# Kernel optimization log

Measured on AMD Instinct MI355X. Metric: run time of the kernel, lower is better.

## Reference

```python
import jax, jax.numpy as jnp
import numpy as np

B, D, N, H = 16384, 8, 64, 128   # batch, input_path_dim, cde_state_dim, vf_hidden_dim
NSIG = D + D * (D - 1) // 2       # Lyndon words up to depth 2: letters + pairs i<j


def setup_inputs() -> dict:
    key = jax.random.key(0)
    ks = jax.random.split(key, 6)
    g = lambda k, shape, scale: jax.random.normal(k, shape, jnp.float32) * scale
    return {
        "h": jax.random.normal(ks[0], (B, N), jnp.float32),
        "primitive_signature": jax.random.normal(ks[1], (B, NSIG), jnp.float32) * 0.1,
        "W1": g(ks[2], (H, N), (1.0 / N) ** 0.5),
        "b1": jnp.zeros((H,), jnp.float32),
        "W2": g(ks[3], (H, H), (1.0 / H) ** 0.5),
        "b2": jnp.zeros((H,), jnp.float32),
        "W3": g(ks[4], (D * N, H), (1.0 / H) ** 0.5),
        "b3": jnp.zeros((D * N,), jnp.float32),
    }


def reference(h, primitive_signature, W1, b1, W2, b2, W3, b3):
    d, n = D, N
    iu, ju = np.triu_indices(d, k=1)  # level-2 Lyndon words ij with i<j, lex order

    def vf(hv):  # MLP vector field: (n,) -> (d, n), one field per input channel
        z = jax.nn.softplus(W1 @ hv + b1)
        z = jax.nn.softplus(W2 @ z + b2)
        return jnp.tanh(W3 @ z + b3).reshape(d, n)

    def single(hv, sig):
        V = vf(hv)  # (d, n) level-1 brackets (the vector fields themselves)
        # JVP of the whole stacked field in direction t: J_{V_j}(h) @ t for all j
        jvp_dir = lambda t: jax.jvp(vf, (hv,), (t,))[1]  # (d, n)
        JV = jax.vmap(jvp_dir)(V)                         # (i, j, n) = J_{V_j} V_i
        # Lie bracket [V_i, V_j](h) = J_{V_j} V_i - J_{V_i} V_j
        br2 = JV - jnp.swapaxes(JV, 0, 1)                 # (i, j, n)
        lyn2 = br2[iu, ju]                                # (d*(d-1)/2, n)
        # log-ODE contraction: sum_w logsig_w * bracket_w(h)
        return sig[:d] @ V + sig[d:] @ lyn2               # (n,)

    return jax.vmap(single)(h, primitive_signature)
```

## Files before the change

kernel.cpp:

```cpp
#include <hip/hip_runtime.h>
#include <hip/hip_bf16.h>

#define NEL 16384

#define W1B_OFF 0
#define W2B_OFF 8192
#define W3B_OFF 24576
#define WS_WEIGHTS 90112
#define S1_OFF  90112
#define S2_OFF  (S1_OFF + NEL*128)
#define Z2_OFF  (S2_OFF + NEL*128)
#define V_OFF   (Z2_OFF + NEL*128)
#define DZ1_OFF (V_OFF + NEL*512)
#define DZ2_OFF (DZ1_OFF + NEL*8*128)

typedef __attribute__((ext_vector_type(8))) short bf16x8;
typedef __attribute__((ext_vector_type(4))) float f32x4;

__device__ __forceinline__ float bf2f(unsigned int u16) {
    unsigned int x = u16 << 16;
    float f; __builtin_memcpy(&f, &x, 4); return f;
}
__device__ __forceinline__ unsigned short f2bf(float f) {
    unsigned int x; __builtin_memcpy(&x, &f, 4);
    x = (x + 0x7FFFu + ((x >> 16) & 1u)) >> 16;
    return (unsigned short)x;
}
__device__ __forceinline__ void unpack8(uint4 q, float* f) {
    f[0] = bf2f(q.x & 0xFFFFu); f[1] = bf2f(q.x >> 16);
    f[2] = bf2f(q.y & 0xFFFFu); f[3] = bf2f(q.y >> 16);
    f[4] = bf2f(q.z & 0xFFFFu); f[5] = bf2f(q.z >> 16);
    f[6] = bf2f(q.w & 0xFFFFu); f[7] = bf2f(q.w >> 16);
}
__device__ __forceinline__ void sp_sig(float x, float& sp, float& sig) {
    float t = __expf(-fabsf(x));
    float r = __builtin_amdgcn_rcpf(1.f + t);
    sig = (x >= 0.f) ? r : 1.f - r;
    sp  = fmaxf(x, 0.f) + __logf(1.f + t);
}
__device__ __forceinline__ float tanh_fast(float x) {
    float t = __expf(-2.f * fabsf(x));
    float y = (1.f - t) * __builtin_amdgcn_rcpf(1.f + t);
    unsigned int xb, yb;
    __builtin_memcpy(&xb, &x, 4);
    __builtin_memcpy(&yb, &y, 4);
    yb |= (xb & 0x80000000u);
    float rr; __builtin_memcpy(&rr, &yb, 4);
    return rr;
}
__device__ __forceinline__ bf16x8 ldfrag(const unsigned short* p) {
    return *reinterpret_cast<const bf16x8*>(p);
}
__device__ __forceinline__ void cpu4(unsigned short* dst, const unsigned short* src) {
    *reinterpret_cast<uint4*>(dst) = *reinterpret_cast<const uint4*>(src);
}

__global__ void prep_weights(const float* __restrict__ W1,
                             const float* __restrict__ W2,
                             const float* __restrict__ W3,
                             unsigned short* __restrict__ wb) {
    int i = blockIdx.x * blockDim.x + threadIdx.x;
    if (i >= WS_WEIGHTS) return;
    float v;
    if (i < W2B_OFF) v = W1[i];
    else if (i < W3B_OFF) v = W2[i - W2B_OFF];
    else v = W3[i - W3B_OFF];
    wb[i] = f2bf(v);
}

#define K1_LDS 52224
__global__ __launch_bounds__(256, 2)
void k1_fwd12(const float* __restrict__ hg,
              const float* __restrict__ b1,
              const float* __restrict__ b2,
              unsigned short* __restrict__ wsb) {
    __shared__ __align__(16) char sm[K1_LDS];
    unsigned short* w1s = (unsigned short*)(sm);
    unsigned short* hs  = (unsigned short*)(sm + 18432);
    unsigned short* w2s = (unsigned short*)(sm);
    unsigned short* z1s = (unsigned short*)(sm + 34816);
    unsigned short* S1g = wsb + S1_OFF;
    unsigned short* S2g = wsb + S2_OFF;
    unsigned short* Z2g = wsb + Z2_OFF;

    const int tid = threadIdx.x;
    const int e0 = blockIdx.x * 64;
    const int lane = tid & 63;
    const int w = tid >> 6;
    const int r16 = lane & 15;
    const int kb = lane >> 4;

    #pragma unroll
    for (int q = 0; q < 4; ++q) {
        int idx = q * 256 + tid;
        int row = idx >> 3, u4 = idx & 7;
        cpu4(&w1s[row * 72 + u4 * 8], &wsb[W1B_OFF + row * 64 + u4 * 8]);
    }
    #pragma unroll
    for (int q = 0; q < 16; ++q) {
        int idx = q * 256 + tid;
        int row = idx >> 6, k = idx & 63;
        hs[row * 72 + k] = f2bf(hg[(e0 + row) * 64 + k]);
    }
    __syncthreads();

    {
        const unsigned short* Ab = hs + (w * 16 + r16) * 72 + kb * 8;
        bf16x8 a0 = ldfrag(Ab), a1 = ldfrag(Ab + 32);
        f32x4 acc[8] = {};
        #pragma unroll
        for (int nt = 0; nt < 8; ++nt) {
            const unsigned short* Bb = w1s + (nt * 16 + r16) * 72 + kb * 8;
            acc[nt] = __builtin_amdgcn_mfma_f32_16x16x32_bf16(a0, ldfrag(Bb), acc[nt], 0, 0, 0);
            acc[nt] = __builtin_amdgcn_mfma_f32_16x16x32_bf16(a1, ldfrag(Bb + 32), acc[nt], 0, 0, 0);
        }
        int rbase = w * 16 + kb * 4;
        #pragma unroll
        for (int nt = 0; nt < 8; ++nt) {
            int col = nt * 16 + r16;
            float bb = b1[col];
            #pragma unroll
            for (int rr = 0; rr < 4; ++rr) {
                float sp, sg;
                sp_sig(acc[nt][rr] + bb, sp, sg);
                z1s[(rbase + rr) * 136 + col] = f2bf(sp);
                S1g[(e0 + rbase + rr) * 128 + col] = f2bf(sg);
            }
        }
    }
    __syncthreads();

    #pragma unroll
    for (int q = 0; q < 8; ++q) {
        int idx = q * 256 + tid;
        int row = idx >> 4, u4 = idx & 15;
        cpu4(&w2s[row * 136 + u4 * 8], &wsb[W2B_OFF + row * 128 + u4 * 8]);
    }
    __syncthreads();

    {
        const unsigned short* Ab = z1s + (w * 16 + r16) * 136 + kb * 8;
        bf16x8 a[4];
        #pragma unroll
        for (int ks = 0; ks < 4; ++ks) a[ks] = ldfrag(Ab + ks * 32);
        f32x4 acc[8] = {};
        #pragma unroll
        for (int nt = 0; nt < 8; ++nt) {
            const unsigned short* Bb = w2s + (nt * 16 + r16) * 136 + kb * 8;
            #pragma unroll
            for (int ks = 0; ks < 4; ++ks)
                acc[nt] = __builtin_amdgcn_mfma_f32_16x16x32_bf16(a[ks], ldfrag(Bb + ks * 32), acc[nt], 0, 0, 0);
        }
        int rbase = w * 16 + kb * 4;
        #pragma unroll
        for (int nt = 0; nt < 8; ++nt) {
            int col = nt * 16 + r16;
            float bb = b2[col];
            #pragma unroll
            for (int rr = 0; rr < 4; ++rr) {
                float sp, sg;
                sp_sig(acc[nt][rr] + bb, sp, sg);
                Z2g[(e0 + rbase + rr) * 128 + col] = f2bf(sp);
                S2g[(e0 + rbase + rr) * 128 + col] = f2bf(sg);
            }
        }
    }
}

#define K2_LDS 52224
__global__ __launch_bounds__(256, 2)
void k2_fwd3(const float* __restrict__ b3,
             unsigned short* __restrict__ wsb) {
    __shared__ __align__(16) char sm[K2_LDS];
    unsigned short* z2s = (unsigned short*)(sm);
    unsigned short* wc  = (unsigned short*)(sm + 17408);
    const unsigned short* Z2g = wsb + Z2_OFF;
    unsigned short* Vg = wsb + V_OFF;

    const int tid = threadIdx.x;
    const int e0 = blockIdx.x * 64;
    const int lane = tid & 63;
    const int w = tid >> 6;
    const int r16 = lane & 15;
    const int kb = lane >> 4;

    #pragma unroll
    for (int q = 0; q < 4; ++q) {
        int idx = q * 256 + tid;
        int row = idx >> 4, u4 = idx & 15;
        cpu4(&z2s[row * 136 + u4 * 8], &Z2g[(e0 + row) * 128 + u4 * 8]);
    }

    for (int nc = 0; nc < 4; ++nc) {
        __syncthreads();
        #pragma unroll
        for (int q = 0; q < 8; ++q) {
            int idx = q * 256 + tid;
            int row = idx >> 4, u4 = idx & 15;
            cpu4(&wc[row * 136 + u4 * 8], &wsb[W3B_OFF + (nc * 128 + row) * 128 + u4 * 8]);
        }
        __syncthreads();

        const unsigned short* Ab = z2s + (w * 16 + r16) * 136 + kb * 8;
        bf16x8 a[4];
        #pragma unroll
        for (int ks = 0; ks < 4; ++ks) a[ks] = ldfrag(Ab + ks * 32);
        f32x4 acc[8] = {};
        #pragma unroll
        for (int nt = 0; nt < 8; ++nt) {
            const unsigned short* Bb = wc + (nt * 16 + r16) * 136 + kb * 8;
            #pragma unroll
            for (int ks = 0; ks < 4; ++ks)
                acc[nt] = __builtin_amdgcn_mfma_f32_16x16x32_bf16(a[ks], ldfrag(Bb + ks * 32), acc[nt], 0, 0, 0);
        }
        int rbase = w * 16 + kb * 4;
        #pragma unroll
        for (int nt = 0; nt < 8; ++nt) {
            int c = nc * 128 + nt * 16 + r16;
            float bb = b3[c];
            #pragma unroll
            for (int rr = 0; rr < 4; ++rr) {
                float v = tanh_fast(acc[nt][rr] + bb);
                Vg[(e0 + rbase + rr) * 512 + c] = f2bf(v);
            }
        }
    }
}

#define K3A_LDS 37120
__global__ __launch_bounds__(256, 4)
void k3a_jvp1(const float* __restrict__ sigg,
              unsigned short* __restrict__ wsb) {
    __shared__ __align__(16) char sm[K3A_LDS];
    unsigned short* vs  = (unsigned short*)(sm);
    unsigned short* w1s = (unsigned short*)(sm + 8320);
    unsigned short* ts  = (unsigned short*)(sm + 26752);
    float* sigsm = (float*)(sm + 35968);
    const unsigned short* S1g = wsb + S1_OFF;
    const unsigned short* Vg  = wsb + V_OFF;
    unsigned short* DZ1g = wsb + DZ1_OFF;

    const int tid = threadIdx.x;
    const int e0 = blockIdx.x * 8;
    const int lane = tid & 63;
    const int w = tid >> 6;
    const int r16 = lane & 15;
    const int kb = lane >> 4;

    #pragma unroll
    for (int q = 0; q < 2; ++q) {
        int idx = q * 256 + tid;
        int row = idx >> 6, u4 = idx & 63;
        cpu4(&vs[row * 520 + u4 * 8], &Vg[(e0 + row) * 512 + u4 * 8]);
    }
    #pragma unroll
    for (int q = 0; q < 4; ++q) {
        int idx = q * 256 + tid;
        int row = idx >> 3, u4 = idx & 7;
        cpu4(&w1s[row * 72 + u4 * 8], &wsb[W1B_OFF + row * 64 + u4 * 8]);
    }
    #pragma unroll
    for (int q = 0; q < 2; ++q) {
        int idx = q * 256 + tid;
        if (idx < 288) sigsm[idx] = sigg[e0 * 36 + idx];
    }
    __syncthreads();

    {
        int m = tid >> 2, kq = tid & 3;
        int e = m >> 3, j = m & 7;
        float c8[8];
        #pragma unroll
        for (int i = 0; i < 8; ++i) {
            float v = 0.f;
            if (i < j) {
                int p = 7 * i - i * (i - 1) / 2 + (j - i - 1);
                v = sigsm[e * 36 + 8 + p];
            } else if (i > j) {
                int p = 7 * j - j * (j - 1) / 2 + (i - j - 1);
                v = -sigsm[e * 36 + 8 + p];
            }
            c8[i] = v;
        }
        float acc[16] = {};
        #pragma unroll
        for (int i = 0; i < 8; ++i) {
            uint4 qa = *reinterpret_cast<const uint4*>(&vs[e * 520 + i * 64 + kq * 16]);
            uint4 qb = *reinterpret_cast<const uint4*>(&vs[e * 520 + i * 64 + kq * 16 + 8]);
            float fa[8], fb[8];
            unpack8(qa, fa); unpack8(qb, fb);
            #pragma unroll
            for (int kk = 0; kk < 8; ++kk) {
                acc[kk]     += c8[i] * fa[kk];
                acc[kk + 8] += c8[i] * fb[kk];
            }
        }
        unsigned short o[16];
        #pragma unroll
        for (int kk = 0; kk < 16; ++kk) o[kk] = f2bf(acc[kk]);
        uint4 qo;
        qo.x = (unsigned int)o[0] | ((unsigned int)o[1] << 16);
        qo.y = (unsigned int)o[2] | ((unsigned int)o[3] << 16);
        qo.z = (unsigned int)o[4] | ((unsigned int)o[5] << 16);
        qo.w = (unsigned int)o[6] | ((unsigned int)o[7] << 16);
        *reinterpret_cast<uint4*>(&ts[m * 72 + kq * 16]) = qo;
        qo.x = (unsigned int)o[8]  | ((unsigned int)o[9]  << 16);
        qo.y = (unsigned int)o[10] | ((unsigned int)o[11] << 16);
        qo.z = (unsigned int)o[12] | ((unsigned int)o[13] << 16);
        qo.w = (unsigned int)o[14] | ((unsigned int)o[15] << 16);
        *reinterpret_cast<uint4*>(&ts[m * 72 + kq * 16 + 8]) = qo;
    }
    __syncthreads();

    {
        const unsigned short* Ab = ts + (w * 16 + r16) * 72 + kb * 8;
        bf16x8 a0 = ldfrag(Ab), a1 = ldfrag(Ab + 32);
        f32x4 acc[8] = {};
        #pragma unroll
        for (int nt = 0; nt < 8; ++nt) {
            const unsigned short* Bb = w1s + (nt * 16 + r16) * 72 + kb * 8;
            acc[nt] = __builtin_amdgcn_mfma_f32_16x16x32_bf16(a0, ldfrag(Bb), acc[nt], 0, 0, 0);
            acc[nt] = __builtin_amdgcn_mfma_f32_16x16x32_bf16(a1, ldfrag(Bb + 32), acc[nt], 0, 0, 0);
        }
        int rbase = w * 16 + kb * 4;
        int e_loc = rbase >> 3;
        #pragma unroll
        for (int nt = 0; nt < 8; ++nt) {
            int col = nt * 16 + r16;
            float s1v = bf2f(S1g[(e0 + e_loc) * 128 + col]);
            #pragma unroll
            for (int rr = 0; rr < 4; ++rr)
                DZ1g[(e0 * 8 + rbase + rr) * 128 + col] = f2bf(acc[nt][rr] * s1v);
        }
    }
}

#define K3B_LDS 52224
__global__ __launch_bounds__(256, 3)
void k3b_jvp2(unsigned short* __restrict__ wsb) {
    __shared__ __align__(16) char sm[K3B_LDS];
    unsigned short* dz1s = (unsigned short*)(sm);
    unsigned short* w2s  = (unsigned short*)(sm + 17408);
    const unsigned short* S2g = wsb + S2_OFF;
    const unsigned short* DZ1g = wsb + DZ1_OFF;
    unsigned short* DZ2g = wsb + DZ2_OFF;

    const int tid = threadIdx.x;
    const int m0 = blockIdx.x * 64;
    const int lane = tid & 63;
    const int w = tid >> 6;
    const int r16 = lane & 15;
    const int kb = lane >> 4;

    #pragma unroll
    for (int q = 0; q < 4; ++q) {
        int idx = q * 256 + tid;
        int row = idx >> 4, u4 = idx & 15;
        cpu4(&dz1s[row * 136 + u4 * 8], &DZ1g[(m0 + row) * 128 + u4 * 8]);
    }
    #pragma unroll
    for (int q = 0; q < 8; ++q) {
        int idx = q * 256 + tid;
        int row = idx >> 4, u4 = idx & 15;
        cpu4(&w2s[row * 136 + u4 * 8], &wsb[W2B_OFF + row * 128 + u4 * 8]);
    }
    __syncthreads();

    const unsigned short* Ab = dz1s + (w * 16 + r16) * 136 + kb * 8;
    bf16x8 a[4];
    #pragma unroll
    for (int ks = 0; ks < 4; ++ks) a[ks] = ldfrag(Ab + ks * 32);
    f32x4 acc[8] = {};
    #pragma unroll
    for (int nt = 0; nt < 8; ++nt) {
        const unsigned short* Bb = w2s + (nt * 16 + r16) * 136 + kb * 8;
        #pragma unroll
        for (int ks = 0; ks < 4; ++ks)
            acc[nt] = __builtin_amdgcn_mfma_f32_16x16x32_bf16(a[ks], ldfrag(Bb + ks * 32), acc[nt], 0, 0, 0);
    }
    int rbase = w * 16 + kb * 4;
    int e_glob = (m0 + rbase) >> 3;
    #pragma unroll
    for (int nt = 0; nt < 8; ++nt) {
        int col = nt * 16 + r16;
        float s2v = bf2f(S2g[e_glob * 128 + col]);
        #pragma unroll
        for (int rr = 0; rr < 4; ++rr)
            DZ2g[(m0 + rbase + rr) * 128 + col] = f2bf(acc[nt][rr] * s2v);
    }
}

#define K4_LDS 37120
__global__ __launch_bounds__(256, 4)
void k4_jvp3(const float* __restrict__ sigg,
             const unsigned short* __restrict__ wsb,
             float* __restrict__ out) {
    __shared__ __align__(16) char sm[K4_LDS];
    unsigned short* adz = (unsigned short*)(sm);
    unsigned short* w3j = (unsigned short*)(sm + 17408);
    float*          sg1 = (float*)(sm + 34816);
    const unsigned short* Vg = wsb + V_OFF;
    const unsigned short* DZ2g = wsb + DZ2_OFF;

    const int tid = threadIdx.x;
    const int e0 = blockIdx.x * 64;
    const int lane = tid & 63;
    const int w = tid >> 6;
    const int r16 = lane & 15;
    const int kb = lane >> 4;
    const int rbase = w * 16 + kb * 4;

    #pragma unroll
    for (int q = 0; q < 2; ++q) {
        int idx = q * 256 + tid;
        int e = idx >> 3, j7 = idx & 7;
        sg1[e * 9 + j7] = sigg[(e0 + e) * 36 + j7];
    }

    float oacc[4][4] = {};

    for (int j = 0; j < 8; ++j) {
        __syncthreads();
        #pragma unroll
        for (int q = 0; q < 4; ++q) {
            int idx = q * 256 + tid;
            int row = idx >> 4, u4 = idx & 15;
            cpu4(&adz[row * 136 + u4 * 8], &DZ2g[((e0 + row) * 8 + j) * 128 + u4 * 8]);
            cpu4(&w3j[row * 136 + u4 * 8], &wsb[W3B_OFF + (j * 64 + row) * 128 + u4 * 8]);
        }
        __syncthreads();

        const unsigned short* Ab = adz + (w * 16 + r16) * 136 + kb * 8;
        bf16x8 a[4];
        #pragma unroll
        for (int ks = 0; ks < 4; ++ks) a[ks] = ldfrag(Ab + ks * 32);
        f32x4 acc[4] = {};
        #pragma unroll
        for (int nt = 0; nt < 4; ++nt) {
            const unsigned short* Bb = w3j + (nt * 16 + r16) * 136 + kb * 8;
            #pragma unroll
            for (int ks = 0; ks < 4; ++ks)
                acc[nt] = __builtin_amdgcn_mfma_f32_16x16x32_bf16(a[ks], ldfrag(Bb + ks * 32), acc[nt], 0, 0, 0);
        }
        #pragma unroll
        for (int nt = 0; nt < 4; ++nt) {
            int np = nt * 16 + r16;
            #pragma unroll
            for (int rr = 0; rr < 4; ++rr) {
                int e = e0 + rbase + rr;
                float v = bf2f(Vg[e * 512 + j * 64 + np]);
                float sv = sg1[(rbase + rr) * 9 + j];
                oacc[nt][rr] += sv * v + (1.f - v * v) * acc[nt][rr];
            }
        }
    }

    #pragma unroll
    for (int nt = 0; nt < 4; ++nt) {
        int np = nt * 16 + r16;
        #pragma unroll
        for (int rr = 0; rr < 4; ++rr)
            out[(e0 + rbase + rr) * 64 + np] = oacc[nt][rr];
    }
}

extern "C" void kernel_launch(void* const* d_in, const int* in_sizes, int n_in,
                              void* d_out, int out_size, void* d_ws, size_t ws_size,
                              hipStream_t stream) {
    const float* hg  = (const float*)d_in[0];
    const float* sg  = (const float*)d_in[1];
    const float* W1  = (const float*)d_in[2];
    const float* b1  = (const float*)d_in[3];
    const float* W2  = (const float*)d_in[4];
    const float* b2  = (const float*)d_in[5];
    const float* W3  = (const float*)d_in[6];
    const float* b3  = (const float*)d_in[7];
    float* outp = (float*)d_out;
    unsigned short* wsb = (unsigned short*)d_ws;

    hipLaunchKernelGGL(prep_weights, dim3((WS_WEIGHTS + 255) / 256), dim3(256), 0, stream,
                       W1, W2, W3, wsb);
    hipLaunchKernelGGL(k1_fwd12, dim3(NEL / 64), dim3(256), 0, stream, hg, b1, b2, wsb);
    hipLaunchKernelGGL(k2_fwd3,  dim3(NEL / 64), dim3(256), 0, stream, b3, wsb);
    hipLaunchKernelGGL(k3a_jvp1, dim3(NEL / 8),  dim3(256), 0, stream, sg, wsb);
    hipLaunchKernelGGL(k3b_jvp2, dim3(NEL * 8 / 64), dim3(256), 0, stream, wsb);
    hipLaunchKernelGGL(k4_jvp3,  dim3(NEL / 64), dim3(256), 0, stream, sg, wsb, outp);
}
```

Baseline: 82.78 us.

## Shrink per-block row tiles and split output columns across waves

Reduces rows per block from 64 to 16 in k1, k2 and k4, and from 64 to 32 in k3b. The four waves now split output column tiles instead of row tiles. This gives 4x (or 2x) more blocks and less LDS per block, and k1/k2 launch bounds rise to 4 blocks per CU, to raise occupancy and parallelism. The cost is that each block reloads the full weight matrices into LDS for fewer rows, so weight traffic and per-block setup grow.

```diff
diff --git a/kernel.cpp b/kernel.cpp
--- a/kernel.cpp
+++ b/kernel.cpp
@@ -68,8 +68,8 @@
     wb[i] = f2bf(v);
 }
 
-#define K1_LDS 52224
-__global__ __launch_bounds__(256, 2)
+#define K1_LDS 39168
+__global__ __launch_bounds__(256, 4)
 void k1_fwd12(const float* __restrict__ hg,
               const float* __restrict__ b1,
               const float* __restrict__ b2,
@@ -84,11 +84,12 @@
     unsigned short* Z2g = wsb + Z2_OFF;
 
     const int tid = threadIdx.x;
-    const int e0 = blockIdx.x * 64;
+    const int e0 = blockIdx.x * 16;
     const int lane = tid & 63;
     const int w = tid >> 6;
     const int r16 = lane & 15;
     const int kb = lane >> 4;
+    const int crow = kb * 4;
 
     #pragma unroll
     for (int q = 0; q < 4; ++q) {
@@ -96,35 +97,38 @@
         int row = idx >> 3, u4 = idx & 7;
         cpu4(&w1s[row * 72 + u4 * 8], &wsb[W1B_OFF + row * 64 + u4 * 8]);
     }
-    #pragma unroll
-    for (int q = 0; q < 16; ++q) {
-        int idx = q * 256 + tid;
-        int row = idx >> 6, k = idx & 63;
-        hs[row * 72 + k] = f2bf(hg[(e0 + row) * 64 + k]);
-    }
-    __syncthreads();
-
-    {
-        const unsigned short* Ab = hs + (w * 16 + r16) * 72 + kb * 8;
+    {
+        int row = tid >> 4, f4 = tid & 15;
+        float4 hv = *reinterpret_cast<const float4*>(&hg[(e0 + row) * 64 + f4 * 4]);
+        ushort2 lo = { f2bf(hv.x), f2bf(hv.y) };
+        ushort2 hi = { f2bf(hv.z), f2bf(hv.w) };
+        *reinterpret_cast<ushort2*>(&hs[row * 72 + f4 * 4]) = lo;
+        *reinterpret_cast<ushort2*>(&hs[row * 72 + f4 * 4 + 2]) = hi;
+    }
+    __syncthreads();
+
+    {
+        const unsigned short* Ab = hs + r16 * 72 + kb * 8;
         bf16x8 a0 = ldfrag(Ab), a1 = ldfrag(Ab + 32);
-        f32x4 acc[8] = {};
-        #pragma unroll
-        for (int nt = 0; nt < 8; ++nt) {
-            const unsigned short* Bb = w1s + (nt * 16 + r16) * 72 + kb * 8;
-            acc[nt] = __builtin_amdgcn_mfma_f32_16x16x32_bf16(a0, ldfrag(Bb), acc[nt], 0, 0, 0);
-            acc[nt] = __builtin_amdgcn_mfma_f32_16x16x32_bf16(a1, ldfrag(Bb + 32), acc[nt], 0, 0, 0);
-        }
-        int rbase = w * 16 + kb * 4;
-        #pragma unroll
-        for (int nt = 0; nt < 8; ++nt) {
-            int col = nt * 16 + r16;
+        f32x4 acc[2] = {};
+        #pragma unroll
+        for (int t = 0; t < 2; ++t) {
+            int col16 = (w * 2 + t) * 16 + r16;
+            const unsigned short* Bb = w1s + col16 * 72 + kb * 8;
+            acc[t] = __builtin_amdgcn_mfma_f32_16x16x32_bf16(a0, ldfrag(Bb), acc[t], 0, 0, 0);
+            acc[t] = __builtin_amdgcn_mfma_f32_16x16x32_bf16(a1, ldfrag(Bb + 32), acc[t], 0, 0, 0);
+        }
+        #pragma unroll
+        for (int t = 0; t < 2; ++t) {
+            int col = (w * 2 + t) * 16 + r16;
             float bb = b1[col];
             #pragma unroll
             for (int rr = 0; rr < 4; ++rr) {
+                int e = crow + rr;
                 float sp, sg;
-                sp_sig(acc[nt][rr] + bb, sp, sg);
-                z1s[(rbase + rr) * 136 + col] = f2bf(sp);
-                S1g[(e0 + rbase + rr) * 128 + col] = f2bf(sg);
+                sp_sig(acc[t][rr] + bb, sp, sg);
+                z1s[e * 136 + col] = f2bf(sp);
+                S1g[(e0 + e) * 128 + col] = f2bf(sg);
             }
         }
     }
@@ -139,55 +143,55 @@
     __syncthreads();
 
     {
-        const unsigned short* Ab = z1s + (w * 16 + r16) * 136 + kb * 8;
+        const unsigned short* Ab = z1s + r16 * 136 + kb * 8;
         bf16x8 a[4];
         #pragma unroll
         for (int ks = 0; ks < 4; ++ks) a[ks] = ldfrag(Ab + ks * 32);
-        f32x4 acc[8] = {};
-        #pragma unroll
-        for (int nt = 0; nt < 8; ++nt) {
-            const unsigned short* Bb = w2s + (nt * 16 + r16) * 136 + kb * 8;
+        f32x4 acc[2] = {};
+        #pragma unroll
+        for (int t = 0; t < 2; ++t) {
+            int col16 = (w * 2 + t) * 16 + r16;
+            const unsigned short* Bb = w2s + col16 * 136 + kb * 8;
             #pragma unroll
             for (int ks = 0; ks < 4; ++ks)
-                acc[nt] = __builtin_amdgcn_mfma_f32_16x16x32_bf16(a[ks], ldfrag(Bb + ks * 32), acc[nt], 0, 0, 0);
-        }
-        int rbase = w * 16 + kb * 4;
-        #pragma unroll
-        for (int nt = 0; nt < 8; ++nt) {
-            int col = nt * 16 + r16;
+                acc[t] = __builtin_amdgcn_mfma_f32_16x16x32_bf16(a[ks], ldfrag(Bb + ks * 32), acc[t], 0, 0, 0);
+        }
+        #pragma unroll
+        for (int t = 0; t < 2; ++t) {
+            int col = (w * 2 + t) * 16 + r16;
             float bb = b2[col];
             #pragma unroll
             for (int rr = 0; rr < 4; ++rr) {
+                int e = crow + rr;
                 float sp, sg;
-                sp_sig(acc[nt][rr] + bb, sp, sg);
-                Z2g[(e0 + rbase + rr) * 128 + col] = f2bf(sp);
-                S2g[(e0 + rbase + rr) * 128 + col] = f2bf(sg);
+                sp_sig(acc[t][rr] + bb, sp, sg);
+                Z2g[(e0 + e) * 128 + col] = f2bf(sp);
+                S2g[(e0 + e) * 128 + col] = f2bf(sg);
             }
         }
     }
 }
 
-#define K2_LDS 52224
-__global__ __launch_bounds__(256, 2)
+#define K2_LDS 39168
+__global__ __launch_bounds__(256, 4)
 void k2_fwd3(const float* __restrict__ b3,
              unsigned short* __restrict__ wsb) {
     __shared__ __align__(16) char sm[K2_LDS];
     unsigned short* z2s = (unsigned short*)(sm);
-    unsigned short* wc  = (unsigned short*)(sm + 17408);
+    unsigned short* wc  = (unsigned short*)(sm + 4352);
     const unsigned short* Z2g = wsb + Z2_OFF;
     unsigned short* Vg = wsb + V_OFF;
 
     const int tid = threadIdx.x;
-    const int e0 = blockIdx.x * 64;
+    const int e0 = blockIdx.x * 16;
     const int lane = tid & 63;
     const int w = tid >> 6;
     const int r16 = lane & 15;
     const int kb = lane >> 4;
-
-    #pragma unroll
-    for (int q = 0; q < 4; ++q) {
-        int idx = q * 256 + tid;
-        int row = idx >> 4, u4 = idx & 15;
+    const int crow = kb * 4;
+
+    {
+        int row = tid >> 4, u4 = tid & 15;
         cpu4(&z2s[row * 136 + u4 * 8], &Z2g[(e0 + row) * 128 + u4 * 8]);
     }
 
@@ -201,27 +205,28 @@
         }
         __syncthreads();
 
-        const unsigned short* Ab = z2s + (w * 16 + r16) * 136 + kb * 8;
+        const unsigned short* Ab = z2s + r16 * 136 + kb * 8;
         bf16x8 a[4];
         #pragma unroll
         for (int ks = 0; ks < 4; ++ks) a[ks] = ldfrag(Ab + ks * 32);
-        f32x4 acc[8] = {};
-        #pragma unroll
-        for (int nt = 0; nt < 8; ++nt) {
-            const unsigned short* Bb = wc + (nt * 16 + r16) * 136 + kb * 8;
+        f32x4 acc[2] = {};
+        #pragma unroll
+        for (int t = 0; t < 2; ++t) {
+            int col16 = (w * 2 + t) * 16 + r16;
+            const unsigned short* Bb = wc + col16 * 136 + kb * 8;
             #pragma unroll
             for (int ks = 0; ks < 4; ++ks)
-                acc[nt] = __builtin_amdgcn_mfma_f32_16x16x32_bf16(a[ks], ldfrag(Bb + ks * 32), acc[nt], 0, 0, 0);
-        }
-        int rbase = w * 16 + kb * 4;
-        #pragma unroll
-        for (int nt = 0; nt < 8; ++nt) {
-            int c = nc * 128 + nt * 16 + r16;
+                acc[t] = __builtin_amdgcn_mfma_f32_16x16x32_bf16(a[ks], ldfrag(Bb + ks * 32), acc[t], 0, 0, 0);
+        }
+        #pragma unroll
+        for (int t = 0; t < 2; ++t) {
+            int c = nc * 128 + (w * 2 + t) * 16 + r16;
             float bb = b3[c];
             #pragma unroll
             for (int rr = 0; rr < 4; ++rr) {
-                float v = tanh_fast(acc[nt][rr] + bb);
-                Vg[(e0 + rbase + rr) * 512 + c] = f2bf(v);
+                int e = crow + rr;
+                float v = tanh_fast(acc[t][rr] + bb);
+                Vg[(e0 + e) * 512 + c] = f2bf(v);
             }
         }
     }
@@ -335,25 +340,26 @@
     }
 }
 
-#define K3B_LDS 52224
+#define K3B_LDS 43520
 __global__ __launch_bounds__(256, 3)
 void k3b_jvp2(unsigned short* __restrict__ wsb) {
     __shared__ __align__(16) char sm[K3B_LDS];
     unsigned short* dz1s = (unsigned short*)(sm);
-    unsigned short* w2s  = (unsigned short*)(sm + 17408);
+    unsigned short* w2s  = (unsigned short*)(sm + 8704);
     const unsigned short* S2g = wsb + S2_OFF;
     const unsigned short* DZ1g = wsb + DZ1_OFF;
     unsigned short* DZ2g = wsb + DZ2_OFF;
 
     const int tid = threadIdx.x;
-    const int m0 = blockIdx.x * 64;
+    const int m0 = blockIdx.x * 32;
     const int lane = tid & 63;
     const int w = tid >> 6;
     const int r16 = lane & 15;
     const int kb = lane >> 4;
-
-    #pragma unroll
-    for (int q = 0; q < 4; ++q) {
+    const int mt = w & 1, nh = w >> 1;
+
+    #pragma unroll
+    for (int q = 0; q < 2; ++q) {
         int idx = q * 256 + tid;
         int row = idx >> 4, u4 = idx & 15;
         cpu4(&dz1s[row * 136 + u4 * 8], &DZ1g[(m0 + row) * 128 + u4 * 8]);
@@ -366,23 +372,23 @@
     }
     __syncthreads();
 
-    const unsigned short* Ab = dz1s + (w * 16 + r16) * 136 + kb * 8;
+    const unsigned short* Ab = dz1s + (mt * 16 + r16) * 136 + kb * 8;
     bf16x8 a[4];
     #pragma unroll
     for (int ks = 0; ks < 4; ++ks) a[ks] = ldfrag(Ab + ks * 32);
-    f32x4 acc[8] = {};
-    #pragma unroll
-    for (int nt = 0; nt < 8; ++nt) {
-        const unsigned short* Bb = w2s + (nt * 16 + r16) * 136 + kb * 8;
+    f32x4 acc[4] = {};
+    #pragma unroll
+    for (int nt = 0; nt < 4; ++nt) {
+        const unsigned short* Bb = w2s + ((nh * 4 + nt) * 16 + r16) * 136 + kb * 8;
         #pragma unroll
         for (int ks = 0; ks < 4; ++ks)
             acc[nt] = __builtin_amdgcn_mfma_f32_16x16x32_bf16(a[ks], ldfrag(Bb + ks * 32), acc[nt], 0, 0, 0);
     }
-    int rbase = w * 16 + kb * 4;
+    int rbase = mt * 16 + kb * 4;
     int e_glob = (m0 + rbase) >> 3;
     #pragma unroll
-    for (int nt = 0; nt < 8; ++nt) {
-        int col = nt * 16 + r16;
+    for (int nt = 0; nt < 4; ++nt) {
+        int col = (nh * 4 + nt) * 16 + r16;
         float s2v = bf2f(S2g[e_glob * 128 + col]);
         #pragma unroll
         for (int rr = 0; rr < 4; ++rr)
@@ -390,78 +396,70 @@
     }
 }
 
-#define K4_LDS 37120
+#define K4_LDS 22336
 __global__ __launch_bounds__(256, 4)
 void k4_jvp3(const float* __restrict__ sigg,
              const unsigned short* __restrict__ wsb,
              float* __restrict__ out) {
     __shared__ __align__(16) char sm[K4_LDS];
     unsigned short* adz = (unsigned short*)(sm);
-    unsigned short* w3j = (unsigned short*)(sm + 17408);
-    float*          sg1 = (float*)(sm + 34816);
+    unsigned short* w3j = (unsigned short*)(sm + 4352);
+    float*          sg1 = (float*)(sm + 21760);
     const unsigned short* Vg = wsb + V_OFF;
     const unsigned short* DZ2g = wsb + DZ2_OFF;
 
     const int tid = threadIdx.x;
-    const int e0 = blockIdx.x * 64;
+    const int e0 = blockIdx.x * 16;
     const int lane = tid & 63;
     const int w = tid >> 6;
     const int r16 = lane & 15;
     const int kb = lane >> 4;
-    const int rbase = w * 16 + kb * 4;
-
-    #pragma unroll
-    for (int q = 0; q < 2; ++q) {
-        int idx = q * 256 + tid;
-        int e = idx >> 3, j7 = idx & 7;
+    const int crow = kb * 4;
+    const int np = w * 16 + r16;
+
+    if (tid < 128) {
+        int e = tid >> 3, j7 = tid & 7;
         sg1[e * 9 + j7] = sigg[(e0 + e) * 36 + j7];
     }
 
-    float oacc[4][4] = {};
+    float oacc[4] = {};
 
     for (int j = 0; j < 8; ++j) {
         __syncthreads();
+        {
+            int row = tid >> 4, u4 = tid & 15;
+            cpu4(&adz[row * 136 + u4 * 8], &DZ2g[((e0 + row) * 8 + j) * 128 + u4 * 8]);
+        }
         #pragma unroll
         for (int q = 0; q < 4; ++q) {
             int idx = q * 256 + tid;
             int row = idx >> 4, u4 = idx & 15;
-            cpu4(&adz[row * 136 + u4 * 8], &DZ2g[((e0 + row) * 8 + j) * 128 + u4 * 8]);
             cpu4(&w3j[row * 136 + u4 * 8], &wsb[W3B_OFF + (j * 64 + row) * 128 + u4 * 8]);
         }
         __syncthreads();
 
-        const unsigned short* Ab = adz + (w * 16 + r16) * 136 + kb * 8;
+        const unsigned short* Ab = adz + r16 * 136 + kb * 8;
         bf16x8 a[4];
         #pragma unroll
         for (int ks = 0; ks < 4; ++ks) a[ks] = ldfrag(Ab + ks * 32);
-        f32x4 acc[4] = {};
-        #pragma unroll
-        for (int nt = 0; nt < 4; ++nt) {
-            const unsigned short* Bb = w3j + (nt * 16 + r16) * 136 + kb * 8;
-            #pragma unroll
-            for (int ks = 0; ks < 4; ++ks)
-                acc[nt] = __builtin_amdgcn_mfma_f32_16x16x32_bf16(a[ks], ldfrag(Bb + ks * 32), acc[nt], 0, 0, 0);
-        }
-        #pragma unroll
-        for (int nt = 0; nt < 4; ++nt) {
-            int np = nt * 16 + r16;
-            #pragma unroll
-            for (int rr = 0; rr < 4; ++rr) {
-                int e = e0 + rbase + rr;
-                float v = bf2f(Vg[e * 512 + j * 64 + np]);
-                float sv = sg1[(rbase + rr) * 9 + j];
-                oacc[nt][rr] += sv * v + (1.f - v * v) * acc[nt][rr];
-            }
-        }
-    }
-
-    #pragma unroll
-    for (int nt = 0; nt < 4; ++nt) {
-        int np = nt * 16 + r16;
-        #pragma unroll
-        for (int rr = 0; rr < 4; ++rr)
-            out[(e0 + rbase + rr) * 64 + np] = oacc[nt][rr];
-    }
+        f32x4 acc = {};
+        const unsigned short* Bb = w3j + np * 136 + kb * 8;
+        #pragma unroll
+        for (int ks = 0; ks < 4; ++ks)
+            acc = __builtin_amdgcn_mfma_f32_16x16x32_bf16(a[ks], ldfrag(Bb + ks * 32), acc, 0, 0, 0);
+
+        #pragma unroll
+        for (int rr = 0; rr < 4; ++rr) {
+            int e = crow + rr;
+            float v = bf2f(Vg[(e0 + e) * 512 + j * 64 + np]);
+            float sv = sg1[e * 9 + j];
+            oacc[rr] += sv * v + (1.f - v * v) * acc[rr];
+        }
+    }
+
+    #pragma unroll
+    for (int rr = 0; rr < 4; ++rr)
+        out[(e0 + crow + rr) * 64 + np] = oacc[rr];
 }
 
 extern "C" void kernel_launch(void* const* d_in, const int* in_sizes, int n_in,
@@ -480,9 +478,9 @@
 
     hipLaunchKernelGGL(prep_weights, dim3((WS_WEIGHTS + 255) / 256), dim3(256), 0, stream,
                        W1, W2, W3, wsb);
-    hipLaunchKernelGGL(k1_fwd12, dim3(NEL / 64), dim3(256), 0, stream, hg, b1, b2, wsb);
-    hipLaunchKernelGGL(k2_fwd3,  dim3(NEL / 64), dim3(256), 0, stream, b3, wsb);
+    hipLaunchKernelGGL(k1_fwd12, dim3(NEL / 16), dim3(256), 0, stream, hg, b1, b2, wsb);
+    hipLaunchKernelGGL(k2_fwd3,  dim3(NEL / 16), dim3(256), 0, stream, b3, wsb);
     hipLaunchKernelGGL(k3a_jvp1, dim3(NEL / 8),  dim3(256), 0, stream, sg, wsb);
-    hipLaunchKernelGGL(k3b_jvp2, dim3(NEL * 8 / 64), dim3(256), 0, stream, wsb);
-    hipLaunchKernelGGL(k4_jvp3,  dim3(NEL / 64), dim3(256), 0, stream, sg, wsb, outp);
-}
+    hipLaunchKernelGGL(k3b_jvp2, dim3(NEL * 8 / 32), dim3(256), 0, stream, wsb);
+    hipLaunchKernelGGL(k4_jvp3,  dim3(NEL / 16), dim3(256), 0, stream, sg, wsb, outp);
+}
```

New measurement: 78.30 us. -5.4%, faster.
